# Optimization experiments

Hardware: AMD Instinct MI355X
Metric: run time of the kernel (lower is better)

The kernel has to match this reference:

```python
import jax, jax.numpy as jnp
import numpy as np


def setup_inputs() -> dict:
    key = jax.random.key(0)
    ks = jax.random.split(key, 8)
    B, L, D = 8, 4096, 1024
    s = 1.0 / np.sqrt(D)  # torch Linear default init scale (approx)
    return {
        "x": jax.random.normal(ks[0], (B, L, D), dtype=jnp.float32),
        "hidden": jax.random.normal(ks[1], (B, D), dtype=jnp.float32),
        "W_f": jax.random.normal(ks[2], (D, D), dtype=jnp.float32) * s,
        "b_f": jnp.zeros((D,), dtype=jnp.float32),
        "W_i": jax.random.normal(ks[3], (D, D), dtype=jnp.float32) * s,
        "b_i": jnp.zeros((D,), dtype=jnp.float32),
        "W_o": jax.random.normal(ks[4], (D, D), dtype=jnp.float32) * s,
        "b_o": jnp.zeros((D,), dtype=jnp.float32),
    }


def reference(x, hidden, W_f, b_f, W_i, b_i, W_o, b_o):
    # x: [B, L, D], hidden: [B, D]
    D = x.shape[-1]
    lin = jnp.linspace(0.0, 1.0, D, dtype=x.dtype)  # per-channel gate scale
    remember = jax.nn.sigmoid(jnp.einsum('bld,ed->ble', x, W_f) + b_f) * lin
    forget = 1.0 - remember
    inp = jnp.tanh(jnp.einsum('bld,ed->ble', x, W_i) + b_i) * remember

    # linear recurrence h_t = forget_t * h_{t-1} + inp_t  via parallel scan
    def combine(c1, c2):
        a1, u1 = c1
        a2, u2 = c2
        return (a1 * a2, a2 * u1 + u2)

    cumprod_forget, h_inner = jax.lax.associative_scan(combine, (forget, inp), axis=1)
    h = h_inner + hidden[:, None, :] * cumprod_forget  # inject initial hidden state
    y = jnp.einsum('bld,ed->ble', h, W_o) + b_o
    return y, h
```

## Files before the change

kernel.cpp:

```cpp
#include <hip/hip_runtime.h>
#include <stdint.h>

#define B_ 8
#define L_ 4096
#define D_ 1024
#define M_ (B_*L_)
#define CHUNKS 128
#define TCH (L_/CHUNKS)

typedef float f32x4 __attribute__((ext_vector_type(4)));
typedef float f32x2 __attribute__((ext_vector_type(2)));
typedef short short8 __attribute__((ext_vector_type(8)));
typedef unsigned short ushort4v __attribute__((ext_vector_type(4)));

static __device__ __forceinline__ unsigned short f2bf(float f) {
  union { float f; unsigned u; } v; v.f = f;
  unsigned r = v.u + 0x7FFFu + ((v.u >> 16) & 1u);
  return (unsigned short)(r >> 16);
}
static __device__ __forceinline__ float bf2f(unsigned short u) {
  union { unsigned u; float f; } v; v.u = ((unsigned)u) << 16; return v.f;
}

#define GLOAD16(g, l) \
  __builtin_amdgcn_global_load_lds((__attribute__((address_space(1))) const void*)(g), \
                                   (__attribute__((address_space(3))) void*)(l), 16, 0, 0)

__global__ __launch_bounds__(256)
void cvt_all(const float* __restrict__ x,  const float* __restrict__ w0,
             const float* __restrict__ w1, const float* __restrict__ w2,
             unsigned short* __restrict__ dst)
{
  const int xn8 = (M_ * D_) / 8;
  const int wn8 = (D_ * D_) / 8;
  int gid = blockIdx.x * 256 + threadIdx.x;
  const float* src;
  size_t soff;
  if (gid < xn8)                { src = x;  soff = (size_t)gid * 8; }
  else if (gid < xn8 + wn8)     { src = w0; soff = (size_t)(gid - xn8) * 8; }
  else if (gid < xn8 + 2 * wn8) { src = w1; soff = (size_t)(gid - xn8 - wn8) * 8; }
  else                          { src = w2; soff = (size_t)(gid - xn8 - 2 * wn8) * 8; }
  const f32x4* s = (const f32x4*)(src + soff);
  f32x4 v0 = s[0], v1 = s[1];
  union { short8 v; unsigned short u[8]; } w;
  w.u[0] = f2bf(v0[0]); w.u[1] = f2bf(v0[1]); w.u[2] = f2bf(v0[2]); w.u[3] = f2bf(v0[3]);
  w.u[4] = f2bf(v1[0]); w.u[5] = f2bf(v1[1]); w.u[6] = f2bf(v1[2]); w.u[7] = f2bf(v1[3]);
  *(short8*)(dst + (size_t)gid * 8) = w.v;
}

template<int MODE>
__global__ __launch_bounds__(512, 2)
void gemm256(const unsigned short* __restrict__ A,
             const unsigned short* __restrict__ Bw,
             const float* __restrict__ bias0,
             const float* __restrict__ bias1,
             unsigned short* __restrict__ ob0,
             unsigned short* __restrict__ ob1,
             float* __restrict__ of)
{
  __shared__ unsigned short lds[81920];
  char* ldsb = (char*)lds;

  const int tid  = threadIdx.x;
  const int lane = tid & 63;
  const int wid  = tid >> 6;
  const int wm   = wid >> 2;
  const int wn   = wid & 3;
  const int frow = lane & 15, ks = lane >> 4;
  const int xsw  = (ks ^ ((frow >> 1) & 3)) << 4;

  constexpr int NBN = (MODE == 0) ? 8 : 4;
  constexpr int GBM = 32 / NBN;
  const int xcd   = blockIdx.x & 7;
  const int slot  = blockIdx.x >> 3;
  const int local = slot & 31;
  const int wrnd  = slot >> 5;
  const int bm = (xcd * 16 + wrnd * GBM + (local & (GBM - 1))) * 256;
  const int bn = (local / GBM) * 256;

  const int r0  = tid >> 2;
  const int scl = ((tid & 3) ^ ((r0 >> 1) & 3)) << 4;
  const char* pA = (const char*)A  + (size_t)(bm + r0) * 2048 + scl;
  const char* pB = (const char*)Bw + (size_t)(bn + r0) * 2048 + scl;
  const int dst16 = tid * 16;

  f32x4 acc[8][4] = {};
  short8 aq[4], bq[4];

  auto stgA = [&](int c, int sl) {
    const char* s = pA + c * 64;
    char* d = ldsb + sl * 16384 + dst16;
    GLOAD16(s,                      d);
    GLOAD16(s + (size_t)128 * 2048, d + 8192);
  };
  auto stgB = [&](int c, int sl) {
    const char* s = pB + c * 64;
    char* d = ldsb + 81920 + sl * 16384 + dst16;
    GLOAD16(s,                      d);
    GLOAD16(s + (size_t)128 * 2048, d + 8192);
  };
  auto ldAB4 = [&](const char* LA, const char* LB) {
    const char* ab = LA + (wm * 128 + frow) * 64 + xsw;
    const char* bb = LB + (wn * 64 + frow) * 64 + xsw;
    aq[0] = *(const short8*)(ab);
    bq[0] = *(const short8*)(bb);
    bq[1] = *(const short8*)(bb + 1024);
    bq[2] = *(const short8*)(bb + 2048);
    bq[3] = *(const short8*)(bb + 3072);
    aq[1] = *(const short8*)(ab + 1024);
    aq[2] = *(const short8*)(ab + 2048);
    aq[3] = *(const short8*)(ab + 3072);
  };
  auto ldA4 = [&](const char* LA) {
    const char* ab = LA + (wm * 128 + 64 + frow) * 64 + xsw;
    aq[0] = *(const short8*)(ab);
    aq[1] = *(const short8*)(ab + 1024);
    aq[2] = *(const short8*)(ab + 2048);
    aq[3] = *(const short8*)(ab + 3072);
  };
  auto mfma16 = [&](int ih) {
    #pragma unroll
    for (int i2 = 0; i2 < 4; ++i2) {
      #pragma unroll
      for (int j = 0; j < 4; ++j)
        acc[ih * 4 + i2][j] =
          __builtin_amdgcn_mfma_f32_16x16x32_bf16(aq[i2], bq[j], acc[ih * 4 + i2][j], 0, 0, 0);
    }
  };

#define BAR __builtin_amdgcn_s_barrier()
#define WAITV(N) asm volatile("s_waitcnt vmcnt(" #N ")" ::: "memory")
#define DO_CH(c, SL, SG, STG, WN)                                             \
  {                                                                           \
    if (STG) { stgA((c) + 4, (SG)); stgB((c) + 4, (SG)); }                    \
    const char* LA = ldsb + (SL) * 16384;                                     \
    const char* LB = ldsb + 81920 + (SL) * 16384;                             \
    ldAB4(LA, LB);                                                            \
    mfma16(0);                                                                \
    ldA4(LA);                                                                 \
    mfma16(1);                                                                \
    WAITV(WN);                                                                \
    BAR;                                                                      \
  }
#define DO_CH_LAST(SL)                                                        \
  {                                                                           \
    const char* LA = ldsb + (SL) * 16384;                                     \
    const char* LB = ldsb + 81920 + (SL) * 16384;                             \
    ldAB4(LA, LB);                                                            \
    mfma16(0);                                                                \
    ldA4(LA);                                                                 \
    mfma16(1);                                                                \
  }

  stgA(0, 0); stgB(0, 0);
  stgA(1, 1); stgB(1, 1);
  stgA(2, 2); stgB(2, 2);
  stgA(3, 3); stgB(3, 3);
  WAITV(12);
  BAR;

  DO_CH( 0, 0, 4, true, 12);
  DO_CH( 1, 1, 0, true, 12);
  DO_CH( 2, 2, 1, true, 12);
  DO_CH( 3, 3, 2, true, 12);
  DO_CH( 4, 4, 3, true, 12);
  DO_CH( 5, 0, 4, true, 12);
  DO_CH( 6, 1, 0, true, 12);
  DO_CH( 7, 2, 1, true, 12);
  DO_CH( 8, 3, 2, true, 12);
  DO_CH( 9, 4, 3, true, 12);
  DO_CH(10, 0, 4, true, 12);
  DO_CH(11, 1, 0, true, 12);
  DO_CH(12, 2, 1, true, 12);
  DO_CH(13, 3, 2, true, 12);
  DO_CH(14, 4, 3, true, 12);
  DO_CH(15, 0, 4, true, 12);
  DO_CH(16, 1, 0, true, 12);
  DO_CH(17, 2, 1, true, 12);
  DO_CH(18, 3, 2, true, 12);
  DO_CH(19, 4, 3, true, 12);
  DO_CH(20, 0, 4, true, 12);
  DO_CH(21, 1, 0, true, 12);
  DO_CH(22, 2, 1, true, 12);
  DO_CH(23, 3, 2, true, 12);
  DO_CH(24, 4, 3, true, 12);
  DO_CH(25, 0, 4, true, 12);
  DO_CH(26, 1, 0, true, 12);
  DO_CH(27, 2, 1, true, 12);
  DO_CH(28, 3, 0, false, 8);
  DO_CH(29, 4, 0, false, 4);
  DO_CH(30, 0, 0, false, 0);
  DO_CH_LAST(1);
#undef DO_CH
#undef DO_CH_LAST
#undef WAITV
#undef BAR

  if constexpr (MODE == 0) {
    const int plane = bn >> 10;
    const int cb    = bn & 1023;
    unsigned short* ob = plane ? ob1 : ob0;
    const float* bs    = plane ? bias1 : bias0;
    float bv[4];
    #pragma unroll
    for (int j = 0; j < 4; ++j) bv[j] = bs[cb + wn * 64 + j * 16 + frow];
    #pragma unroll
    for (int ii = 0; ii < 8; ++ii) {
      int row = bm + wm * 128 + ii * 16 + ks * 4;
      #pragma unroll
      for (int j = 0; j < 4; ++j) {
        int col = cb + wn * 64 + j * 16 + frow;
        float lin = (float)col * (1.0f / 1023.0f);
        #pragma unroll
        for (int r = 0; r < 4; ++r) {
          float z = acc[ii][j][r] + bv[j];
          float v;
          if (plane == 0) {
            v = lin / (1.0f + __expf(-z));
          } else {
            float e2 = __expf(2.0f * z);
            v = 1.0f - 2.0f / (e2 + 1.0f);
          }
          ob[(size_t)(row + r) * D_ + col] = f2bf(v);
        }
      }
    }
  } else {
    float bv[4];
    #pragma unroll
    for (int j = 0; j < 4; ++j) bv[j] = bias0[bn + wn * 64 + j * 16 + frow];
    #pragma unroll
    for (int ii = 0; ii < 8; ++ii) {
      int row = bm + wm * 128 + ii * 16 + ks * 4;
      #pragma unroll
      for (int j = 0; j < 4; ++j) {
        int col = bn + wn * 64 + j * 16 + frow;
        #pragma unroll
        for (int r = 0; r < 4; ++r)
          of[(size_t)(row + r) * D_ + col] = acc[ii][j][r] + bv[j];
      }
    }
  }
}

__global__ __launch_bounds__(256)
void scan_partial_b(const unsigned short* __restrict__ rb,
                    const unsigned short* __restrict__ tb,
                    float* __restrict__ Ag, float* __restrict__ Ug)
{
  int blk = blockIdx.x;
  int b = blk >> 7, c = blk & (CHUNKS - 1);
  int e = threadIdx.x << 2;
  size_t base = ((size_t)b * L_ + (size_t)c * TCH) * D_ + e;
  f32x4 a = {1.f,1.f,1.f,1.f}, u = {0.f,0.f,0.f,0.f};
  for (int t = 0; t < TCH; ++t) {
    ushort4v r4 = *(const ushort4v*)(rb + base + (size_t)t * D_);
    ushort4v t4 = *(const ushort4v*)(tb + base + (size_t)t * D_);
    #pragma unroll
    for (int j = 0; j < 4; ++j) {
      float rem = bf2f(r4[j]);
      float f   = 1.0f - rem;
      float inp = bf2f(t4[j]) * rem;
      u[j] = fmaf(f, u[j], inp);
      a[j] *= f;
    }
  }
  size_t o = (size_t)(b * CHUNKS + c) * D_ + e;
  *(f32x4*)(Ag + o) = a;
  *(f32x4*)(Ug + o) = u;
}

__global__ __launch_bounds__(256)
void scan_carry(const float* __restrict__ Ag, const float* __restrict__ Ug,
                const float* __restrict__ hidden, float* __restrict__ Hin)
{
  int gid = blockIdx.x * 256 + threadIdx.x;
  int b = gid >> 8;
  int e = (gid & 255) << 2;
  f32x4 h = *(const f32x4*)(hidden + (size_t)b * D_ + e);
  for (int c = 0; c < CHUNKS; ++c) {
    size_t o = (size_t)(b * CHUNKS + c) * D_ + e;
    *(f32x4*)(Hin + o) = h;
    f32x4 A = *(const f32x4*)(Ag + o);
    f32x4 U = *(const f32x4*)(Ug + o);
    h = A * h + U;
  }
}

__global__ __launch_bounds__(256)
void scan_apply_b(const unsigned short* __restrict__ rb,
                  const unsigned short* __restrict__ tb,
                  const float* __restrict__ Hin,
                  float* __restrict__ hout, unsigned short* __restrict__ hb)
{
  int blk = blockIdx.x;
  int b = blk >> 7, c = blk & (CHUNKS - 1);
  int e = threadIdx.x << 2;
  size_t base = ((size_t)b * L_ + (size_t)c * TCH) * D_ + e;
  f32x4 h = *(const f32x4*)(Hin + (size_t)(b * CHUNKS + c) * D_ + e);
  for (int t = 0; t < TCH; ++t) {
    size_t o = base + (size_t)t * D_;
    ushort4v r4 = *(const ushort4v*)(rb + o);
    ushort4v t4 = *(const ushort4v*)(tb + o);
    #pragma unroll
    for (int j = 0; j < 4; ++j) {
      float rem = bf2f(r4[j]);
      float f   = 1.0f - rem;
      float inp = bf2f(t4[j]) * rem;
      h[j] = fmaf(f, h[j], inp);
    }
    *(f32x4*)(hout + o) = h;
    ushort4v p;
    p[0] = f2bf(h[0]); p[1] = f2bf(h[1]); p[2] = f2bf(h[2]); p[3] = f2bf(h[3]);
    *(ushort4v*)(hb + o) = p;
  }
}

template<int MODE>
__global__ __launch_bounds__(256, 2)
void gemm_slow(const float* __restrict__ A, const float* __restrict__ B0,
               const float* __restrict__ B1, const float* __restrict__ bias0,
               const float* __restrict__ bias1, float* __restrict__ out0,
               float* __restrict__ out1)
{
  constexpr int BK = 32;
  __shared__ unsigned short As[128 * BK];
  __shared__ unsigned short Bs0[128 * BK];
  __shared__ unsigned short Bs1[(MODE == 0) ? (128 * BK) : 8];

  const int tid = threadIdx.x, lane = tid & 63, wave = tid >> 6;
  const int wr = wave >> 1, wc = wave & 1;
  const int bm = blockIdx.x * 128, bn = blockIdx.y * 128;
  f32x4 acc0[4][4] = {};
  f32x4 acc1[(MODE == 0) ? 4 : 1][(MODE == 0) ? 4 : 1] = {};
  const int frow = lane & 15, kslot = lane >> 4;
  const int xs = kslot ^ (frow & 3);

  auto stage = [&](const float* src, unsigned short* dst) {
    #pragma unroll
    for (int p = 0; p < 4; ++p) {
      int g = p * 256 + tid;
      int row = g >> 3, kq = (g & 7) << 2;
      f32x4 v = *(const f32x4*)(src + (size_t)row * D_ + kq);
      ushort4v w;
      w[0] = f2bf(v[0]); w[1] = f2bf(v[1]); w[2] = f2bf(v[2]); w[3] = f2bf(v[3]);
      int byte = kq << 1, slot = byte >> 4, sub = byte & 15;
      int off = row * 64 + ((slot ^ (row & 3)) << 4) + sub;
      *(ushort4v*)((char*)dst + off) = w;
    }
  };

  for (int k0 = 0; k0 < D_; k0 += BK) {
    stage(A + (size_t)bm * D_ + k0, As);
    stage(B0 + (size_t)bn * D_ + k0, Bs0);
    if constexpr (MODE == 0) stage(B1 + (size_t)bn * D_ + k0, Bs1);
    __syncthreads();
    short8 af[4], bf0[4], bf1[4];
    #pragma unroll
    for (int i = 0; i < 4; ++i) {
      int ar = wr * 64 + i * 16 + frow;
      af[i] = *(const short8*)((const char*)As + ar * 64 + (xs << 4));
      int br = wc * 64 + i * 16 + frow;
      bf0[i] = *(const short8*)((const char*)Bs0 + br * 64 + (xs << 4));
      if constexpr (MODE == 0)
        bf1[i] = *(const short8*)((const char*)Bs1 + br * 64 + (xs << 4));
    }
    #pragma unroll
    for (int i = 0; i < 4; ++i)
      #pragma unroll
      for (int j = 0; j < 4; ++j) {
        acc0[i][j] = __builtin_amdgcn_mfma_f32_16x16x32_bf16(af[i], bf0[j], acc0[i][j], 0, 0, 0);
        if constexpr (MODE == 0)
          acc1[i][j] = __builtin_amdgcn_mfma_f32_16x16x32_bf16(af[i], bf1[j], acc1[i][j], 0, 0, 0);
      }
    __syncthreads();
  }
  #pragma unroll
  for (int i = 0; i < 4; ++i)
    #pragma unroll
    for (int j = 0; j < 4; ++j)
      #pragma unroll
      for (int r = 0; r < 4; ++r) {
        int row = bm + wr * 64 + i * 16 + (lane >> 4) * 4 + r;
        int col = bn + wc * 64 + j * 16 + (lane & 15);
        size_t idx = (size_t)row * D_ + col;
        if constexpr (MODE == 0) {
          float zf = acc0[i][j][r] + bias0[col];
          float linv = (float)col * (1.0f / 1023.0f);
          float rem = linv / (1.0f + __expf(-zf));
          float zi = acc1[i][j][r] + bias1[col];
          float e2 = __expf(2.0f * zi);
          float th = 1.0f - 2.0f / (e2 + 1.0f);
          out0[idx] = 1.0f - rem;
          out1[idx] = th * rem;
        } else {
          out0[idx] = acc0[i][j][r] + bias0[col];
        }
      }
}

__global__ __launch_bounds__(256)
void scan_partial_f(const float* __restrict__ p0, const float* __restrict__ p1,
                    float* __restrict__ Ag, float* __restrict__ Ug)
{
  int blk = blockIdx.x;
  int b = blk / (CHUNKS * 2);
  int c = (blk >> 1) & (CHUNKS - 1);
  int e = ((blk & 1) << 9) + threadIdx.x * 2;
  size_t base = ((size_t)b * L_ + (size_t)c * TCH) * D_ + e;
  f32x2 a = {1.0f, 1.0f}, u = {0.0f, 0.0f};
  for (int t = 0; t < TCH; ++t) {
    f32x2 f = *(const f32x2*)(p0 + base + (size_t)t * D_);
    f32x2 i = *(const f32x2*)(p1 + base + (size_t)t * D_);
    u = f * u + i;
    a = a * f;
  }
  size_t o = (size_t)(b * CHUNKS + c) * D_ + e;
  *(f32x2*)(Ag + o) = a;
  *(f32x2*)(Ug + o) = u;
}

__global__ __launch_bounds__(256)
void scan_apply_f(const float* __restrict__ p0, float* __restrict__ p1_io,
                  const float* __restrict__ Hin)
{
  int blk = blockIdx.x;
  int b = blk / (CHUNKS * 2);
  int c = (blk >> 1) & (CHUNKS - 1);
  int e = ((blk & 1) << 9) + threadIdx.x * 2;
  size_t base = ((size_t)b * L_ + (size_t)c * TCH) * D_ + e;
  f32x2 h = *(const f32x2*)(Hin + (size_t)(b * CHUNKS + c) * D_ + e);
  for (int t = 0; t < TCH; ++t) {
    size_t o = base + (size_t)t * D_;
    f32x2 f = *(const f32x2*)(p0 + o);
    f32x2 i = *(const f32x2*)(p1_io + o);
    h = f * h + i;
    *(f32x2*)(p1_io + o) = h;
  }
}

extern "C" void kernel_launch(void* const* d_in, const int* in_sizes, int n_in,
                              void* d_out, int out_size, void* d_ws, size_t ws_size,
                              hipStream_t stream)
{
  const float* x      = (const float*)d_in[0];
  const float* hidden = (const float*)d_in[1];
  const float* W_f    = (const float*)d_in[2];
  const float* b_f    = (const float*)d_in[3];
  const float* W_i    = (const float*)d_in[4];
  const float* b_i    = (const float*)d_in[5];
  const float* W_o    = (const float*)d_in[6];
  const float* b_o    = (const float*)d_in[7];

  float* y = (float*)d_out;
  float* h = y + (size_t)M_ * D_;

  const size_t xb_elems = (size_t)M_ * D_;
  const size_t w_elems  = (size_t)D_ * D_;
  const size_t agg      = (size_t)B_ * CHUNKS * D_;
  const size_t need = (xb_elems * 3 + 3 * w_elems) * 2 + agg * 3 * 4;

  if (ws_size >= need) {
    unsigned short* xb  = (unsigned short*)d_ws;
    unsigned short* wfb = xb + xb_elems;
    unsigned short* wib = wfb + w_elems;
    unsigned short* wob = wib + w_elems;
    unsigned short* rbv = wob + w_elems;
    unsigned short* tbv = rbv + xb_elems;
    float* Ag  = (float*)(tbv + xb_elems);
    float* Ug  = Ag + agg;
    float* Hin = Ug + agg;

    int cblk = (int)((xb_elems + 3 * w_elems) / 8 / 256);
    cvt_all<<<cblk, 256, 0, stream>>>(x, W_f, W_i, W_o, xb);

    gemm256<0><<<1024, 512, 0, stream>>>(xb, wfb, b_f, b_i, rbv, tbv, nullptr);

    int pblocks = B_ * CHUNKS;
    scan_partial_b<<<pblocks, 256, 0, stream>>>(rbv, tbv, Ag, Ug);
    scan_carry<<<(B_ * D_ / 4) / 256, 256, 0, stream>>>(Ag, Ug, hidden, Hin);
    scan_apply_b<<<pblocks, 256, 0, stream>>>(rbv, tbv, Hin, h, xb);

    gemm256<1><<<512, 512, 0, stream>>>(xb, wob, b_o, nullptr, nullptr, nullptr, y);
  } else {
    float* Ag  = (float*)d_ws;
    float* Ug  = Ag + agg;
    float* Hin = Ug + agg;
    dim3 gg(M_ / 128, D_ / 128);
    int pblocks = B_ * CHUNKS * 2;

    gemm_slow<0><<<gg, 256, 0, stream>>>(x, W_f, W_i, b_f, b_i, y, h);
    scan_partial_f<<<pblocks, 256, 0, stream>>>(y, h, Ag, Ug);
    scan_carry<<<(B_ * D_ / 4) / 256, 256, 0, stream>>>(Ag, Ug, hidden, Hin);
    scan_apply_f<<<pblocks, 256, 0, stream>>>(y, h, Hin);
    gemm_slow<1><<<gg, 256, 0, stream>>>(h, W_o, nullptr, b_o, nullptr, y, nullptr);
  }
}
```

Before: 390.9 us.

## Load GEMM B-operand fragments directly from global into registers, halving LDS

The GEMM no longer stages the weight (B) tile through LDS. Each wave loads its B fragments straight from global memory into a triple-buffered register set, prefetched two K-chunks ahead, while A remains staged in LDS. This halves LDS usage and removes the B LDS reads and writes, which could allow higher occupancy. In exchange, each of the four row-waves now reads B redundantly from global/L2, register pressure rises, and the vmcnt wait counts change.

```diff
diff --git a/kernel.cpp b/kernel.cpp
--- a/kernel.cpp
+++ b/kernel.cpp
@@ -50,15 +50,15 @@
 
 template<int MODE>
 __global__ __launch_bounds__(512, 2)
-void gemm256(const unsigned short* __restrict__ A,
-             const unsigned short* __restrict__ Bw,
-             const float* __restrict__ bias0,
-             const float* __restrict__ bias1,
-             unsigned short* __restrict__ ob0,
-             unsigned short* __restrict__ ob1,
-             float* __restrict__ of)
-{
-  __shared__ unsigned short lds[81920];
+void gemmBR(const unsigned short* __restrict__ A,
+            const unsigned short* __restrict__ Bw,
+            const float* __restrict__ bias0,
+            const float* __restrict__ bias1,
+            unsigned short* __restrict__ ob0,
+            unsigned short* __restrict__ ob1,
+            float* __restrict__ of)
+{
+  __shared__ unsigned short lds[40960];
   char* ldsb = (char*)lds;
 
   const int tid  = threadIdx.x;
@@ -80,12 +80,16 @@
 
   const int r0  = tid >> 2;
   const int scl = ((tid & 3) ^ ((r0 >> 1) & 3)) << 4;
-  const char* pA = (const char*)A  + (size_t)(bm + r0) * 2048 + scl;
-  const char* pB = (const char*)Bw + (size_t)(bn + r0) * 2048 + scl;
+  const char* pA = (const char*)A + (size_t)(bm + r0) * 2048 + scl;
   const int dst16 = tid * 16;
 
+  const char* pBf = (const char*)Bw + (size_t)(bn + wn * 64 + frow) * 2048 + ks * 16;
+
   f32x4 acc[8][4] = {};
-  short8 aq[4], bq[4];
+  short8 aq[8];
+  short8 bqA0, bqA1, bqA2, bqA3;
+  short8 bqB0, bqB1, bqB2, bqB3;
+  short8 bqC0, bqC1, bqC2, bqC3;
 
   auto stgA = [&](int c, int sl) {
     const char* s = pA + c * 64;
@@ -93,107 +97,89 @@
     GLOAD16(s,                      d);
     GLOAD16(s + (size_t)128 * 2048, d + 8192);
   };
-  auto stgB = [&](int c, int sl) {
-    const char* s = pB + c * 64;
-    char* d = ldsb + 81920 + sl * 16384 + dst16;
-    GLOAD16(s,                      d);
-    GLOAD16(s + (size_t)128 * 2048, d + 8192);
-  };
-  auto ldAB4 = [&](const char* LA, const char* LB) {
-    const char* ab = LA + (wm * 128 + frow) * 64 + xsw;
-    const char* bb = LB + (wn * 64 + frow) * 64 + xsw;
-    aq[0] = *(const short8*)(ab);
-    bq[0] = *(const short8*)(bb);
-    bq[1] = *(const short8*)(bb + 1024);
-    bq[2] = *(const short8*)(bb + 2048);
-    bq[3] = *(const short8*)(bb + 3072);
-    aq[1] = *(const short8*)(ab + 1024);
-    aq[2] = *(const short8*)(ab + 2048);
-    aq[3] = *(const short8*)(ab + 3072);
-  };
-  auto ldA4 = [&](const char* LA) {
-    const char* ab = LA + (wm * 128 + 64 + frow) * 64 + xsw;
+  auto ldA8 = [&](int sl) {
+    const char* ab = ldsb + sl * 16384 + (wm * 128 + frow) * 64 + xsw;
     aq[0] = *(const short8*)(ab);
     aq[1] = *(const short8*)(ab + 1024);
     aq[2] = *(const short8*)(ab + 2048);
     aq[3] = *(const short8*)(ab + 3072);
+    aq[4] = *(const short8*)(ab + 4096);
+    aq[5] = *(const short8*)(ab + 5120);
+    aq[6] = *(const short8*)(ab + 6144);
+    aq[7] = *(const short8*)(ab + 7168);
   };
-  auto mfma16 = [&](int ih) {
-    #pragma unroll
-    for (int i2 = 0; i2 < 4; ++i2) {
-      #pragma unroll
-      for (int j = 0; j < 4; ++j)
-        acc[ih * 4 + i2][j] =
-          __builtin_amdgcn_mfma_f32_16x16x32_bf16(aq[i2], bq[j], acc[ih * 4 + i2][j], 0, 0, 0);
-    }
-  };
-
+
+#define LDB(S, c)                                                             \
+  {                                                                           \
+    const char* bp = pBf + (size_t)(c) * 64;                                  \
+    S##0 = *(const short8*)(bp);                                              \
+    S##1 = *(const short8*)(bp + 32768);                                      \
+    S##2 = *(const short8*)(bp + 65536);                                      \
+    S##3 = *(const short8*)(bp + 98304);                                      \
+  }
+#define MFMA32(S)                                                             \
+  {                                                                           \
+    _Pragma("unroll")                                                         \
+    for (int i = 0; i < 8; ++i) {                                             \
+      acc[i][0] = __builtin_amdgcn_mfma_f32_16x16x32_bf16(aq[i], S##0, acc[i][0], 0, 0, 0); \
+      acc[i][1] = __builtin_amdgcn_mfma_f32_16x16x32_bf16(aq[i], S##1, acc[i][1], 0, 0, 0); \
+      acc[i][2] = __builtin_amdgcn_mfma_f32_16x16x32_bf16(aq[i], S##2, acc[i][2], 0, 0, 0); \
+      acc[i][3] = __builtin_amdgcn_mfma_f32_16x16x32_bf16(aq[i], S##3, acc[i][3], 0, 0, 0); \
+    }                                                                         \
+  }
 #define BAR __builtin_amdgcn_s_barrier()
-#define WAITV(N) asm volatile("s_waitcnt vmcnt(" #N ")" ::: "memory")
-#define DO_CH(c, SL, SG, STG, WN)                                             \
+#define DO_CH(SL, SGA, USE, LSET, c, STGA, DOLB, WN)                          \
   {                                                                           \
-    if (STG) { stgA((c) + 4, (SG)); stgB((c) + 4, (SG)); }                    \
-    const char* LA = ldsb + (SL) * 16384;                                     \
-    const char* LB = ldsb + 81920 + (SL) * 16384;                             \
-    ldAB4(LA, LB);                                                            \
-    mfma16(0);                                                                \
-    ldA4(LA);                                                                 \
-    mfma16(1);                                                                \
-    WAITV(WN);                                                                \
+    if (DOLB) LDB(LSET, (c) + 2);                                             \
+    if (STGA) stgA((c) + 4, (SGA));                                           \
+    ldA8(SL);                                                                 \
+    MFMA32(USE);                                                              \
+    asm volatile("s_waitcnt vmcnt(" #WN ")" ::: "memory");                    \
     BAR;                                                                      \
   }
-#define DO_CH_LAST(SL)                                                        \
-  {                                                                           \
-    const char* LA = ldsb + (SL) * 16384;                                     \
-    const char* LB = ldsb + 81920 + (SL) * 16384;                             \
-    ldAB4(LA, LB);                                                            \
-    mfma16(0);                                                                \
-    ldA4(LA);                                                                 \
-    mfma16(1);                                                                \
-  }
-
-  stgA(0, 0); stgB(0, 0);
-  stgA(1, 1); stgB(1, 1);
-  stgA(2, 2); stgB(2, 2);
-  stgA(3, 3); stgB(3, 3);
-  WAITV(12);
+
+  stgA(0, 0); stgA(1, 1); stgA(2, 2); stgA(3, 3);
+  LDB(bqA, 0);
+  LDB(bqB, 1);
+  asm volatile("s_waitcnt vmcnt(4)" ::: "memory");
   BAR;
 
-  DO_CH( 0, 0, 4, true, 12);
-  DO_CH( 1, 1, 0, true, 12);
-  DO_CH( 2, 2, 1, true, 12);
-  DO_CH( 3, 3, 2, true, 12);
-  DO_CH( 4, 4, 3, true, 12);
-  DO_CH( 5, 0, 4, true, 12);
-  DO_CH( 6, 1, 0, true, 12);
-  DO_CH( 7, 2, 1, true, 12);
-  DO_CH( 8, 3, 2, true, 12);
-  DO_CH( 9, 4, 3, true, 12);
-  DO_CH(10, 0, 4, true, 12);
-  DO_CH(11, 1, 0, true, 12);
-  DO_CH(12, 2, 1, true, 12);
-  DO_CH(13, 3, 2, true, 12);
-  DO_CH(14, 4, 3, true, 12);
-  DO_CH(15, 0, 4, true, 12);
-  DO_CH(16, 1, 0, true, 12);
-  DO_CH(17, 2, 1, true, 12);
-  DO_CH(18, 3, 2, true, 12);
-  DO_CH(19, 4, 3, true, 12);
-  DO_CH(20, 0, 4, true, 12);
-  DO_CH(21, 1, 0, true, 12);
-  DO_CH(22, 2, 1, true, 12);
-  DO_CH(23, 3, 2, true, 12);
-  DO_CH(24, 4, 3, true, 12);
-  DO_CH(25, 0, 4, true, 12);
-  DO_CH(26, 1, 0, true, 12);
-  DO_CH(27, 2, 1, true, 12);
-  DO_CH(28, 3, 0, false, 8);
-  DO_CH(29, 4, 0, false, 4);
-  DO_CH(30, 0, 0, false, 0);
-  DO_CH_LAST(1);
+  DO_CH( 0, 4, bqA, bqC,  0, true,  true, 18);
+  DO_CH( 1, 0, bqB, bqA,  1, true,  true, 18);
+  DO_CH( 2, 1, bqC, bqB,  2, true,  true, 18);
+  DO_CH( 3, 2, bqA, bqC,  3, true,  true, 18);
+  DO_CH( 4, 3, bqB, bqA,  4, true,  true, 18);
+  DO_CH( 0, 4, bqC, bqB,  5, true,  true, 18);
+  DO_CH( 1, 0, bqA, bqC,  6, true,  true, 18);
+  DO_CH( 2, 1, bqB, bqA,  7, true,  true, 18);
+  DO_CH( 3, 2, bqC, bqB,  8, true,  true, 18);
+  DO_CH( 4, 3, bqA, bqC,  9, true,  true, 18);
+  DO_CH( 0, 4, bqB, bqA, 10, true,  true, 18);
+  DO_CH( 1, 0, bqC, bqB, 11, true,  true, 18);
+  DO_CH( 2, 1, bqA, bqC, 12, true,  true, 18);
+  DO_CH( 3, 2, bqB, bqA, 13, true,  true, 18);
+  DO_CH( 4, 3, bqC, bqB, 14, true,  true, 18);
+  DO_CH( 0, 4, bqA, bqC, 15, true,  true, 18);
+  DO_CH( 1, 0, bqB, bqA, 16, true,  true, 18);
+  DO_CH( 2, 1, bqC, bqB, 17, true,  true, 18);
+  DO_CH( 3, 2, bqA, bqC, 18, true,  true, 18);
+  DO_CH( 4, 3, bqB, bqA, 19, true,  true, 18);
+  DO_CH( 0, 4, bqC, bqB, 20, true,  true, 18);
+  DO_CH( 1, 0, bqA, bqC, 21, true,  true, 18);
+  DO_CH( 2, 1, bqB, bqA, 22, true,  true, 18);
+  DO_CH( 3, 2, bqC, bqB, 23, true,  true, 18);
+  DO_CH( 4, 3, bqA, bqC, 24, true,  true, 18);
+  DO_CH( 0, 4, bqB, bqA, 25, true,  true, 18);
+  DO_CH( 1, 0, bqC, bqB, 26, true,  true, 18);
+  DO_CH( 2, 1, bqA, bqC, 27, true,  true, 18);
+  DO_CH( 3, 0, bqB, bqA, 28, false, true, 16);
+  DO_CH( 4, 0, bqC, bqB, 29, false, true, 14);
+  DO_CH( 0, 0, bqA, bqA, 30, false, false, 8);
+  ldA8(1);
+  MFMA32(bqB);
 #undef DO_CH
-#undef DO_CH_LAST
-#undef WAITV
+#undef MFMA32
+#undef LDB
 #undef BAR
 
   if constexpr (MODE == 0) {
@@ -474,14 +460,14 @@
     int cblk = (int)((xb_elems + 3 * w_elems) / 8 / 256);
     cvt_all<<<cblk, 256, 0, stream>>>(x, W_f, W_i, W_o, xb);
 
-    gemm256<0><<<1024, 512, 0, stream>>>(xb, wfb, b_f, b_i, rbv, tbv, nullptr);
+    gemmBR<0><<<1024, 512, 0, stream>>>(xb, wfb, b_f, b_i, rbv, tbv, nullptr);
 
     int pblocks = B_ * CHUNKS;
     scan_partial_b<<<pblocks, 256, 0, stream>>>(rbv, tbv, Ag, Ug);
     scan_carry<<<(B_ * D_ / 4) / 256, 256, 0, stream>>>(Ag, Ug, hidden, Hin);
     scan_apply_b<<<pblocks, 256, 0, stream>>>(rbv, tbv, Hin, h, xb);
 
-    gemm256<1><<<512, 512, 0, stream>>>(xb, wob, b_o, nullptr, nullptr, nullptr, y);
+    gemmBR<1><<<512, 512, 0, stream>>>(xb, wob, b_o, nullptr, nullptr, nullptr, y);
   } else {
     float* Ag  = (float*)d_ws;
     float* Ug  = Ag + agg;
```

Measured after the change: 455.6 us. 16.6% more time.
